# Kernel optimization log

Measured on AMD Instinct MI355X. Metric: run time of the kernel, lower is better.

## Reference

```python
import jax, jax.numpy as jnp
import numpy as np

EMBED = 32
HIDDEN = 128
BATCH = 512
SEQ = 512


def setup_inputs() -> dict:
    key = jax.random.key(0)
    k_x, k_wx, k_wh = jax.random.split(key, 3)
    stdu = 1.0 / np.sqrt(HIDDEN)
    x = jax.random.normal(k_x, (BATCH, SEQ, EMBED), dtype=jnp.float32)
    W_x = jax.random.uniform(k_wx, (EMBED, HIDDEN), minval=-stdu, maxval=stdu, dtype=jnp.float32)
    W_h = jax.random.uniform(k_wh, (HIDDEN, HIDDEN), minval=-stdu, maxval=stdu, dtype=jnp.float32)
    b_h = jnp.zeros((HIDDEN,), dtype=jnp.float32)
    return {"x": x, "W_x": W_x, "W_h": W_h, "b_h": b_h}


def reference(x, W_x, W_h, b_h):
    # Elman RNN: h_t = tanh(x_t @ W_x + h_{t-1} @ W_h + b_h)
    B = x.shape[0]
    h0 = jnp.zeros((B, HIDDEN), dtype=x.dtype)
    # Precompute the input projection for all timesteps (same math as per-step matmul)
    xW = jnp.einsum('bte,eh->bth', x, W_x)  # [B, T, H]

    def step(h, xw_t):
        h = jnp.tanh(xw_t + h @ W_h + b_h)
        return h, h

    h_final, out_seq = jax.lax.scan(step, h0, xW.transpose(1, 0, 2))  # out_seq: [T, B, H]
    out = out_seq.transpose(1, 0, 2)  # [B, T, H] (batch_first, like pad_packed output)
    return out, h_final
```

## Files before the change

kernel.cpp:

```cpp
#include <hip/hip_runtime.h>

#define T_SEQ 512
#define EMB 32
#define HID 128
#define BB 2
#define LDSW 160
#define PF 4
#define GROWS 64

typedef __attribute__((ext_vector_type(8))) short short8;
typedef __attribute__((ext_vector_type(4))) float f32x4;

__device__ __forceinline__ short f2bf(float f) {
  union { float f; unsigned u; } v; v.f = f;
  unsigned r = (v.u + 0x7FFFu + ((v.u >> 16) & 1u)) >> 16;
  return (short)r;
}

__device__ __forceinline__ float bf2f(unsigned short u) {
  union { unsigned u; float f; } c; c.u = ((unsigned)u) << 16; return c.f;
}

__device__ __forceinline__ float tanh_fast(float a) {
  float e = __expf(2.0f * a);
  return 1.0f - 2.0f * __builtin_amdgcn_rcpf(e + 1.0f);
}

#define MFMA(a, b, c) __builtin_amdgcn_mfma_f32_16x16x32_bf16((a), (b), (c), 0, 0, 0)

__global__ __launch_bounds__(256) void xw_gemm_kernel(
    const float* __restrict__ x, const float* __restrict__ Wx,
    const float* __restrict__ bh, unsigned short* __restrict__ xw) {
  const int tid = threadIdx.x;
  const int wid = tid >> 6;
  const int lane = tid & 63;
  const int l4 = lane >> 4, lm = lane & 15;
  const int colbase = wid * 32;

  short8 wxf[2]; float bv[2];
#pragma unroll
  for (int nt = 0; nt < 2; ++nt) {
    const int col = colbase + 16 * nt + lm;
    bv[nt] = bh[col];
    short8 fx;
#pragma unroll
    for (int j = 0; j < 8; ++j)
      fx[j] = f2bf(Wx[(size_t)(8 * l4 + j) * HID + col]);
    wxf[nt] = fx;
  }

  const size_t row0 = (size_t)blockIdx.x * GROWS;
#pragma unroll
  for (int mt = 0; mt < GROWS / 16; ++mt) {
    const size_t arow = row0 + mt * 16 + lm;
    const float* xp = x + arow * EMB + 8 * l4;
    f32x4 xf0 = *(const f32x4*)xp;
    f32x4 xf1 = *(const f32x4*)(xp + 4);
    short8 xa;
#pragma unroll
    for (int j = 0; j < 4; ++j) { xa[j] = f2bf(xf0[j]); xa[4 + j] = f2bf(xf1[j]); }
    f32x4 acc0 = {bv[0], bv[0], bv[0], bv[0]};
    f32x4 acc1 = {bv[1], bv[1], bv[1], bv[1]};
    acc0 = MFMA(xa, wxf[0], acc0);
    acc1 = MFMA(xa, wxf[1], acc1);
    unsigned short* op = xw + (row0 + mt * 16 + 4 * l4) * HID;
#pragma unroll
    for (int r = 0; r < 4; ++r) {
      op[(size_t)r * HID + colbase + lm]      = (unsigned short)f2bf(acc0[r]);
      op[(size_t)r * HID + colbase + 16 + lm] = (unsigned short)f2bf(acc1[r]);
    }
  }
}

__global__ __launch_bounds__(256) void rnn_rec_kernel(
    const unsigned short* __restrict__ xw, const float* __restrict__ Wh,
    float* __restrict__ out) {
  __shared__ short hbuf[2][BB][LDSW];

  const int tid = threadIdx.x;
  const int wid = tid >> 6;
  const int lane = tid & 63;
  const int l4 = lane >> 4, lm = lane & 15;
  const int row0 = blockIdx.x * BB;
  const int colbase = wid * 32;

  for (int i = tid; i < 2 * BB * LDSW; i += 256) ((short*)hbuf)[i] = 0;

  short8 whf[2][4];
#pragma unroll
  for (int nt = 0; nt < 2; ++nt) {
    const int col = colbase + 16 * nt + lm;
#pragma unroll
    for (int kb = 0; kb < 4; ++kb) {
      short8 f;
#pragma unroll
      for (int j = 0; j < 8; ++j)
        f[j] = f2bf(Wh[(size_t)(32 * kb + 8 * l4 + j) * HID + col]);
      whf[nt][kb] = f;
    }
  }

  const int rsel = l4 & 1;
  const int csel = l4 >> 1;
  const int ocol = colbase + 16 * csel + lm;

  const unsigned xw_off0  = ((unsigned)(row0 + rsel) * T_SEQ) * (HID * 2) + (unsigned)ocol * 2;
  const unsigned out_off0 = ((unsigned)(row0 + rsel) * T_SEQ) * (HID * 4) + (unsigned)ocol * 4;
  const unsigned short* xwb = xw;
  float* outb = out;
  float* hfinp = out + (size_t)512 * T_SEQ * HID + (size_t)(row0 + rsel) * HID + ocol;

  const short* hr0 = &hbuf[0][lm & 1][8 * l4];
  const short* hr1 = &hbuf[1][lm & 1][8 * l4];
  short* hw0 = &hbuf[0][rsel][ocol];
  short* hw1 = &hbuf[1][rsel][ocol];

  unsigned xr0, xr1, xr2, xr3;
  asm volatile("global_load_ushort %0, %1, %2" : "=v"(xr0) : "v"(xw_off0 + 0u * 256u), "s"(xwb));
  asm volatile("global_load_ushort %0, %1, %2" : "=v"(xr1) : "v"(xw_off0 + 1u * 256u), "s"(xwb));
  asm volatile("global_load_ushort %0, %1, %2" : "=v"(xr2) : "v"(xw_off0 + 2u * 256u), "s"(xwb));
  asm volatile("global_load_ushort %0, %1, %2" : "=v"(xr3) : "v"(xw_off0 + 3u * 256u), "s"(xwb));

  float th_last = 0.f;

  __syncthreads();

#define RSTEP(T, PAR, WN, XR) do {                                               \
    const short* hb_ = (PAR) ? hr0 : hr1;                      \
    short8 ah0 = *(const short8*)(hb_ + 0);                                      \
    short8 ah1 = *(const short8*)(hb_ + 32);                                     \
    short8 ah2 = *(const short8*)(hb_ + 64);                                     \
    short8 ah3 = *(const short8*)(hb_ + 96);                                     \
    unsigned xv_;                                                                \
    asm volatile("s_waitcnt vmcnt(" #WN ")\n\tv_mov_b32 %0, %1"                  \
                 : "=&v"(xv_) : "v"(XR));                                        \
    int tl_ = (T) + PF; if (tl_ > T_SEQ - 1) tl_ = T_SEQ - 1;                    \
    asm volatile("global_load_ushort %0, %1, %2"                                 \
                 : "=v"(XR) : "v"(xw_off0 + (unsigned)tl_ * 256u), "s"(xwb));    \
    const f32x4 z_ = {0.f, 0.f, 0.f, 0.f};                                       \
    f32x4 a0 = MFMA(ah0, whf[0][0], z_);                                         \
    f32x4 a1 = MFMA(ah0, whf[1][0], z_);                                         \
    f32x4 b0 = MFMA(ah2, whf[0][2], z_);                                         \
    f32x4 b1 = MFMA(ah2, whf[1][2], z_);                                         \
    a0 = MFMA(ah1, whf[0][1], a0);                                               \
    a1 = MFMA(ah1, whf[1][1], a1);                                               \
    b0 = MFMA(ah3, whf[0][3], b0);                                               \
    b1 = MFMA(ah3, whf[1][3], b1);                                               \
    float vA0 = rsel ? a0[1] : a0[0];                                            \
    float vB0 = rsel ? b0[1] : b0[0];                                            \
    float vA1 = rsel ? a1[1] : a1[0];                                            \
    float vB1 = rsel ? b1[1] : b1[0];                                            \
    float v_ = (csel ? (vA1 + vB1) : (vA0 + vB0)) + bf2f((unsigned short)xv_);   \
    float th_ = tanh_fast(v_);                                                   \
    *((PAR) ? hw1 : hw0) = f2bf(th_);                             \
    asm volatile("global_store_dword %0, %1, %2"                                 \
                 :: "v"(out_off0 + (unsigned)(T) * 512u), "v"(th_), "s"(outb));  \
    th_last = th_;                                                               \
    asm volatile("s_waitcnt lgkmcnt(0)\n\ts_barrier" ::: "memory");              \
  } while (0)

  RSTEP(0, 0, 3, xr0);
  RSTEP(1, 1, 4, xr1);
  RSTEP(2, 0, 5, xr2);
  RSTEP(3, 1, 6, xr3);
  for (int tb = 4; tb < T_SEQ; tb += 4) {
    RSTEP(tb + 0, 0, 7, xr0);
    RSTEP(tb + 1, 1, 7, xr1);
    RSTEP(tb + 2, 0, 7, xr2);
    RSTEP(tb + 3, 1, 7, xr3);
  }
#undef RSTEP

  *hfinp = th_last;
}

__global__ __launch_bounds__(256) void rnn_fused_fallback(
    const float* __restrict__ x, const float* __restrict__ Wx,
    const float* __restrict__ Wh, const float* __restrict__ bh,
    float* __restrict__ out) {
  __shared__ short hbuf[2][BB][LDSW];
  const int tid = threadIdx.x;
  const int wid = tid >> 6;
  const int lane = tid & 63;
  const int l4 = lane >> 4, lm = lane & 15;
  const int row0 = blockIdx.x * BB;
  const int colbase = wid * 32;
  for (int i = tid; i < 2 * BB * LDSW; i += 256) ((short*)hbuf)[i] = 0;
  short8 whf[2][4]; short8 wxf[2]; float bv[2];
#pragma unroll
  for (int nt = 0; nt < 2; ++nt) {
    const int col = colbase + 16 * nt + lm;
    bv[nt] = bh[col];
#pragma unroll
    for (int kb = 0; kb < 4; ++kb) {
      short8 f;
#pragma unroll
      for (int j = 0; j < 8; ++j)
        f[j] = f2bf(Wh[(size_t)(32 * kb + 8 * l4 + j) * HID + col]);
      whf[nt][kb] = f;
    }
    short8 fx;
#pragma unroll
    for (int j = 0; j < 8; ++j)
      fx[j] = f2bf(Wx[(size_t)(8 * l4 + j) * HID + col]);
    wxf[nt] = fx;
  }
  const int xrow = row0 + (lm & 1);
  const float* xptr = x + (size_t)xrow * T_SEQ * EMB + 8 * l4;
  f32x4 xf0 = *(const f32x4*)(xptr);
  f32x4 xf1 = *(const f32x4*)(xptr + 4);
  const int rsel = l4 & 1, csel = l4 >> 1;
  const int ocol = colbase + 16 * csel + lm;
  float* outp = out + (size_t)(row0 + rsel) * T_SEQ * HID + ocol;
  float* hfinp = out + (size_t)512 * T_SEQ * HID + (size_t)(row0 + rsel) * HID + ocol;
  __syncthreads();
#pragma unroll 2
  for (int t = 0; t < T_SEQ; ++t) {
    const int cur = t & 1, prev = cur ^ 1;
    const short* hb = &hbuf[prev][lm & 1][0];
    short8 ah[4];
#pragma unroll
    for (int kb = 0; kb < 4; ++kb)
      ah[kb] = *(const short8*)(hb + 32 * kb + 8 * l4);
    short8 xa;
#pragma unroll
    for (int j = 0; j < 4; ++j) { xa[j] = f2bf(xf0[j]); xa[4 + j] = f2bf(xf1[j]); }
    if (t + 1 < T_SEQ) {
      xf0 = *(const f32x4*)(xptr + (size_t)(t + 1) * EMB);
      xf1 = *(const f32x4*)(xptr + (size_t)(t + 1) * EMB + 4);
    }
    f32x4 acc0a = {bv[0], bv[0], bv[0], bv[0]};
    f32x4 acc1a = {bv[1], bv[1], bv[1], bv[1]};
    f32x4 acc0b = {0.f, 0.f, 0.f, 0.f};
    f32x4 acc1b = {0.f, 0.f, 0.f, 0.f};
    acc0a = MFMA(xa, wxf[0], acc0a);
    acc1a = MFMA(xa, wxf[1], acc1a);
    acc0a = MFMA(ah[0], whf[0][0], acc0a);
    acc1a = MFMA(ah[0], whf[1][0], acc1a);
    acc0a = MFMA(ah[1], whf[0][1], acc0a);
    acc1a = MFMA(ah[1], whf[1][1], acc1a);
    acc0b = MFMA(ah[2], whf[0][2], acc0b);
    acc1b = MFMA(ah[2], whf[1][2], acc1b);
    acc0b = MFMA(ah[3], whf[0][3], acc0b);
    acc1b = MFMA(ah[3], whf[1][3], acc1b);
    float v0 = (rsel ? acc0a[1] : acc0a[0]) + (rsel ? acc0b[1] : acc0b[0]);
    float v1 = (rsel ? acc1a[1] : acc1a[0]) + (rsel ? acc1b[1] : acc1b[0]);
    float v = csel ? v1 : v0;
    float th = tanh_fast(v);
    hbuf[cur][rsel][ocol] = f2bf(th);
    *outp = th; outp += HID;
    if (t == T_SEQ - 1) *hfinp = th;
    asm volatile("s_waitcnt lgkmcnt(0)\n\ts_barrier" ::: "memory");
  }
}

extern "C" void kernel_launch(void* const* d_in, const int* in_sizes, int n_in,
                              void* d_out, int out_size, void* d_ws, size_t ws_size,
                              hipStream_t stream) {
  const float* x  = (const float*)d_in[0];
  const float* Wx = (const float*)d_in[1];
  const float* Wh = (const float*)d_in[2];
  const float* bh = (const float*)d_in[3];
  float* out = (float*)d_out;
  (void)in_sizes; (void)n_in; (void)out_size;

  const size_t need = (size_t)512 * T_SEQ * HID * sizeof(unsigned short);
  if (ws_size >= need) {
    unsigned short* xw = (unsigned short*)d_ws;
    xw_gemm_kernel<<<(512 * T_SEQ) / GROWS, 256, 0, stream>>>(x, Wx, bh, xw);
    rnn_rec_kernel<<<512 / BB, 256, 0, stream>>>(xw, Wh, out);
  } else {
    rnn_fused_fallback<<<512 / BB, 256, 0, stream>>>(x, Wx, Wh, bh, out);
  }
}
```

Baseline: 140.5 us.

## Process one batch row per block in the recurrent kernel

The recurrent kernel now gives each block a single batch row instead of two, which doubles the grid to 512 blocks and shrinks the LDS hidden-state buffer. The per-step result selection is simpler, since lanes no longer pick between two rows. The aim is to put more independent recurrence chains on each CU so their step latencies can overlap. In exchange the 16-row MFMA tiles carry more wasted rows, two blocks compete for the same CU's matrix units, and the row-select lanes now store duplicate values.

New measurement: 143.7 us. +2.2%, slower.

```diff
diff --git a/kernel.cpp b/kernel.cpp
--- a/kernel.cpp
+++ b/kernel.cpp
@@ -3,7 +3,6 @@
 #define T_SEQ 512
 #define EMB 32
 #define HID 128
-#define BB 2
 #define LDSW 160
 #define PF 4
 #define GROWS 64
@@ -75,16 +74,16 @@
 __global__ __launch_bounds__(256) void rnn_rec_kernel(
     const unsigned short* __restrict__ xw, const float* __restrict__ Wh,
     float* __restrict__ out) {
-  __shared__ short hbuf[2][BB][LDSW];
+  __shared__ short hbuf[2][LDSW];
 
   const int tid = threadIdx.x;
   const int wid = tid >> 6;
   const int lane = tid & 63;
   const int l4 = lane >> 4, lm = lane & 15;
-  const int row0 = blockIdx.x * BB;
+  const int row0 = blockIdx.x;
   const int colbase = wid * 32;
 
-  for (int i = tid; i < 2 * BB * LDSW; i += 256) ((short*)hbuf)[i] = 0;
+  for (int i = tid; i < 2 * LDSW; i += 256) ((short*)hbuf)[i] = 0;
 
   short8 whf[2][4];
 #pragma unroll
@@ -100,20 +99,19 @@
     }
   }
 
-  const int rsel = l4 & 1;
   const int csel = l4 >> 1;
   const int ocol = colbase + 16 * csel + lm;
 
-  const unsigned xw_off0  = ((unsigned)(row0 + rsel) * T_SEQ) * (HID * 2) + (unsigned)ocol * 2;
-  const unsigned out_off0 = ((unsigned)(row0 + rsel) * T_SEQ) * (HID * 4) + (unsigned)ocol * 4;
+  const unsigned xw_off0  = ((unsigned)row0 * T_SEQ) * (HID * 2) + (unsigned)ocol * 2;
+  const unsigned out_off0 = ((unsigned)row0 * T_SEQ) * (HID * 4) + (unsigned)ocol * 4;
   const unsigned short* xwb = xw;
   float* outb = out;
-  float* hfinp = out + (size_t)512 * T_SEQ * HID + (size_t)(row0 + rsel) * HID + ocol;
-
-  const short* hr0 = &hbuf[0][lm & 1][8 * l4];
-  const short* hr1 = &hbuf[1][lm & 1][8 * l4];
-  short* hw0 = &hbuf[0][rsel][ocol];
-  short* hw1 = &hbuf[1][rsel][ocol];
+  float* hfinp = out + (size_t)512 * T_SEQ * HID + (size_t)row0 * HID + ocol;
+
+  const short* hr0 = &hbuf[0][8 * l4];
+  const short* hr1 = &hbuf[1][8 * l4];
+  short* hw0 = &hbuf[0][ocol];
+  short* hw1 = &hbuf[1][ocol];
 
   unsigned xr0, xr1, xr2, xr3;
   asm volatile("global_load_ushort %0, %1, %2" : "=v"(xr0) : "v"(xw_off0 + 0u * 256u), "s"(xwb));
@@ -146,13 +144,11 @@
     a1 = MFMA(ah1, whf[1][1], a1);                                               \
     b0 = MFMA(ah3, whf[0][3], b0);                                               \
     b1 = MFMA(ah3, whf[1][3], b1);                                               \
-    float vA0 = rsel ? a0[1] : a0[0];                                            \
-    float vB0 = rsel ? b0[1] : b0[0];                                            \
-    float vA1 = rsel ? a1[1] : a1[0];                                            \
-    float vB1 = rsel ? b1[1] : b1[0];                                            \
-    float v_ = (csel ? (vA1 + vB1) : (vA0 + vB0)) + bf2f((unsigned short)xv_);   \
+    float s0_ = a0[0] + b0[0];                 \
+    float s1_ = a1[0] + b1[0];                                                   \
+    float v_ = (csel ? s1_ : s0_) + bf2f((unsigned short)xv_);                   \
     float th_ = tanh_fast(v_);                                                   \
-    *((PAR) ? hw1 : hw0) = f2bf(th_);                             \
+    *((PAR) ? hw1 : hw0) = f2bf(th_);             \
     asm volatile("global_store_dword %0, %1, %2"                                 \
                  :: "v"(out_off0 + (unsigned)(T) * 512u), "v"(th_), "s"(outb));  \
     th_last = th_;                                                               \
@@ -178,14 +174,14 @@
     const float* __restrict__ x, const float* __restrict__ Wx,
     const float* __restrict__ Wh, const float* __restrict__ bh,
     float* __restrict__ out) {
-  __shared__ short hbuf[2][BB][LDSW];
+  __shared__ short hbuf[2][2][LDSW];
   const int tid = threadIdx.x;
   const int wid = tid >> 6;
   const int lane = tid & 63;
   const int l4 = lane >> 4, lm = lane & 15;
-  const int row0 = blockIdx.x * BB;
+  const int row0 = blockIdx.x * 2;
   const int colbase = wid * 32;
-  for (int i = tid; i < 2 * BB * LDSW; i += 256) ((short*)hbuf)[i] = 0;
+  for (int i = tid; i < 2 * 2 * LDSW; i += 256) ((short*)hbuf)[i] = 0;
   short8 whf[2][4]; short8 wxf[2]; float bv[2];
 #pragma unroll
   for (int nt = 0; nt < 2; ++nt) {
@@ -268,8 +264,8 @@
   if (ws_size >= need) {
     unsigned short* xw = (unsigned short*)d_ws;
     xw_gemm_kernel<<<(512 * T_SEQ) / GROWS, 256, 0, stream>>>(x, Wx, bh, xw);
-    rnn_rec_kernel<<<512 / BB, 256, 0, stream>>>(xw, Wh, out);
+    rnn_rec_kernel<<<512, 256, 0, stream>>>(xw, Wh, out);
   } else {
-    rnn_fused_fallback<<<512 / BB, 256, 0, stream>>>(x, Wx, Wh, bh, out);
-  }
-}
+    rnn_fused_fallback<<<256, 256, 0, stream>>>(x, Wx, Wh, bh, out);
+  }
+}
```
